# Kernel tuning notes

Hardware: AMD Instinct MI355X
Metric: run time of the kernel (lower is better)

## Reference

```python
import jax, jax.numpy as jnp
import numpy as np

V = 50000      # vocab (embedding table has V+1 rows)
EMB = 256      # emb_dim
E = 128        # rnn_hidden_size (encoder_size)
B, QL, PL, AL = 8, 128, 256, 10


def gru_dir(x, Wih, Whh, bih, bhh, reverse):
    """Single-direction GRU with PyTorch gate math. x: [B,T,I] -> [B,T,H]."""
    pre = jnp.einsum('bti,gi->btg', x, Wih) + bih  # input projection done once: [B,T,3H]
    if reverse:
        pre = pre[:, ::-1]
    H = Whh.shape[1]
    def step(h, p):
        gh = h @ Whh.T + bhh
        r = jax.nn.sigmoid(p[:, :H] + gh[:, :H])
        z = jax.nn.sigmoid(p[:, H:2 * H] + gh[:, H:2 * H])
        n = jnp.tanh(p[:, 2 * H:] + r * gh[:, 2 * H:])
        h_new = (1.0 - z) * n + z * h
        return h_new, h_new
    h0 = jnp.zeros((x.shape[0], H), x.dtype)
    _, hs = jax.lax.scan(step, h0, jnp.swapaxes(pre, 0, 1))
    hs = jnp.swapaxes(hs, 0, 1)
    return hs[:, ::-1] if reverse else hs


def bigru(x, Wih, Whh, bih, bhh):
    f = gru_dir(x, Wih[0], Whh[0], bih[0], bhh[0], False)
    b = gru_dir(x, Wih[1], Whh[1], bih[1], bhh[1], True)
    return jnp.concatenate([f, b], axis=-1)


def setup_inputs() -> dict:
    key = jax.random.key(0)
    ks = iter(jax.random.split(key, 64))
    u = lambda shape, s: jax.random.uniform(next(ks), shape, jnp.float32, -s, s)
    def gru_params(inp, hid):
        s = 1.0 / np.sqrt(hid)
        return (u((2, 3 * hid, inp), s), u((2, 3 * hid, hid), s),
                u((2, 3 * hid), s), u((2, 3 * hid), s))
    d = {}
    d['emb'] = u((V + 1, EMB), 0.1)
    d['a_att'] = u((1, EMB), 0.05)
    for name, (o, i) in {'Wc1': (E, 2 * E), 'Wc2': (E, 2 * E), 'vc': (1, E),
                         'Wb': (2 * E, 2 * E), 'Wd': (E, 2 * E), 'vd': (1, E),
                         'Wm': (E, 2 * E), 'vm': (1, E), 'Ws': (E, 2 * E), 'vs': (1, E),
                         'Wq': (E, 2 * E), 'vq': (1, E), 'Wp1': (E, 2 * E), 'Wp2': (E, 2 * E),
                         'vp': (1, E), 'Wpred': (EMB, 2 * E)}.items():
        d[name] = u((o, i), 0.05)
    d['q_Wih'], d['q_Whh'], d['q_bih'], d['q_bhh'] = gru_params(EMB, E)
    d['p_Wih'], d['p_Whh'], d['p_bih'], d['p_bhh'] = gru_params(EMB, E)
    d['a_Wih'], d['a_Whh'], d['a_bih'], d['a_bhh'] = gru_params(EMB, EMB // 2)
    d['g_Wih'], d['g_Whh'], d['g_bih'], d['g_bhh'] = gru_params(12 * E, E)
    d['query'] = jax.random.randint(next(ks), (B, QL), 0, V)
    d['passage'] = jax.random.randint(next(ks), (B, PL), 0, V)
    d['candidate_neg'] = jax.random.randint(next(ks), (B, AL), 0, V)
    d['candidate_pos'] = jax.random.randint(next(ks), (B, AL), 0, V)
    d['candidate_na'] = jax.random.randint(next(ks), (B, AL), 0, V)
    return d


def reference(emb, a_att, Wc1, Wc2, vc, Wb, Wd, vd, Wm, vm, Ws, vs, Wq, vq, Wp1, Wp2, vp, Wpred,
              q_Wih, q_Whh, q_bih, q_bhh, p_Wih, p_Whh, p_bih, p_bhh,
              a_Wih, a_Whh, a_bih, a_bhh, g_Wih, g_Whh, g_bih, g_bhh,
              query, passage, candidate_neg, candidate_pos, candidate_na):
    def cand_out(ids):
        h = bigru(emb[ids], a_Wih, a_Whh, a_bih, a_bhh)   # [B,A,EMB]
        s = jax.nn.softmax(h @ a_att.T, axis=1)           # softmax over candidate tokens
        return jnp.sum(s * h, axis=1)                     # [B,EMB]
    a_emb = jnp.stack([cand_out(candidate_neg), cand_out(candidate_pos), cand_out(candidate_na)], axis=1)

    # NOTE: source swaps inputs -- q_encoder consumes the passage and vice versa.
    hq = bigru(emb[passage], q_Wih, q_Whh, q_bih, q_bhh)  # [B,P,2E]
    hp = bigru(emb[query], p_Wih, p_Whh, p_bih, p_bhh)    # [B,Q,2E]

    # concat (additive) attention
    sc = jnp.tanh((hq @ Wc1.T)[:, None, :, :] + (hp @ Wc2.T)[:, :, None, :])  # [B,Q,P,E]
    ait = jax.nn.softmax(jnp.einsum('bqpe,e->bqp', sc, vc[0]), axis=-1)
    qtc = jnp.einsum('bqp,bpe->bqe', ait, hq)
    # bilinear attention
    ait = jax.nn.softmax(jnp.einsum('bqe,bpe->bqp', hp, hq @ Wb.T), axis=-1)
    qtb = jnp.einsum('bqp,bpe->bqe', ait, hq)
    # elementwise-product (dot) attention
    prod = hq[:, None, :, :] * hp[:, :, None, :]          # [B,Q,P,2E]
    sd = jnp.tanh(jnp.einsum('bqpf,ef->bqpe', prod, Wd))
    ait = jax.nn.softmax(jnp.einsum('bqpe,e->bqp', sd, vd[0]), axis=-1)
    qtd = jnp.einsum('bqp,bpe->bqe', ait, hq)
    # difference (minus) attention
    diff = hq[:, None, :, :] - hp[:, :, None, :]
    sm = jnp.tanh(jnp.einsum('bqpf,ef->bqpe', diff, Wm))
    ait = jax.nn.softmax(jnp.einsum('bqpe,e->bqp', sm, vm[0]), axis=-1)
    qtm = jnp.einsum('bqp,bpe->bqe', ait, hq)
    # self attention over hp
    sp = hp[:, None, :, :] * hp[:, :, None, :]            # [B,Q,Q,2E]
    ss = jnp.tanh(jnp.einsum('bqkf,ef->bqke', sp, Ws))
    ait = jax.nn.softmax(jnp.einsum('bqke,e->bqk', ss, vs[0]), axis=-1)
    qts = jnp.einsum('bqk,bke->bqe', ait, hp)

    agg = jnp.concatenate([hp, qts, qtc, qtd, qtb, qtm], axis=-1)  # [B,Q,12E]
    agg_rep = bigru(agg, g_Wih, g_Whh, g_bih, g_bhh)               # [B,Q,2E]

    # prediction layer
    sj = jax.nn.softmax(jnp.einsum('bpe,e->bp', jnp.tanh(hq @ Wq.T), vq[0]), axis=-1)
    rq = jnp.einsum('bp,bpe->be', sj, hq)                          # [B,2E]
    # NB: source has no tanh here (vp(Wp1(agg)+Wp2(rq)))
    sj2 = jax.nn.softmax(jnp.einsum('bqe,e->bq', agg_rep @ Wp1.T + (rq @ Wp2.T)[:, None, :], vp[0]), axis=-1)
    rp = jnp.einsum('bq,bqe->be', sj2, agg_rep)                    # [B,2E]
    enc_out = jax.nn.leaky_relu(rp @ Wpred.T)                      # [B,EMB], slope 0.01 as in torch
    logits = jnp.einsum('bce,be->bc', a_emb, enc_out)              # [B,3]
    return logits
```

## Files before the change

### kernel.cpp

```cpp
#include <hip/hip_runtime.h>
#include <hip/hip_bf16.h>


#define BB 8
#define QL 128
#define PL 256
#define AL 10
#define EE 128
#define EMB 256
#define G3 384
#define HH 128

#define O_XPASS   ((size_t)0)
#define O_XQUERY  ((size_t)524288)
#define O_XCAND   ((size_t)786432)
#define O_PREQ    ((size_t)847872)
#define O_PREP    ((size_t)2420736)
#define O_PREA    ((size_t)3207168)
#define O_PREG    ((size_t)3391488)
#define O_HQ      ((size_t)4177920)
#define O_HP      ((size_t)4702208)
#define O_HCAND   ((size_t)4964352)
#define O_AEMB    ((size_t)5025792)
#define O_AQ      ((size_t)5031936)
#define O_AP      ((size_t)5294080)
#define O_BQ      ((size_t)5425152)
#define O_AGG     ((size_t)5949440)
#define O_AGGREP  ((size_t)7522304)
#define O_CQ      ((size_t)7784448)
#define O_GP      ((size_t)8046592)
#define O_RQ      ((size_t)8177664)
#define O_RQW     ((size_t)8179712)
#define O_RP      ((size_t)8180736)
#define O_SCD0    O_XPASS
#define O_SCD1    (O_XPASS + (size_t)262144)
#define O_MQ2     O_PREQ
#define O_MP2     (O_PREQ + (size_t)262144)
#define O_SCS0    O_PREP
#define O_SCS1    (O_PREP + (size_t)131072)

typedef __attribute__((ext_vector_type(8))) short bf16x8;
typedef __attribute__((ext_vector_type(4))) float f32x4;
typedef __attribute__((ext_vector_type(2))) float v2f;
union U4 { uint4 u; bf16x8 v; };

#define BAR_LDS() asm volatile("s_waitcnt lgkmcnt(0)\n\ts_barrier" ::: "memory")

__device__ __forceinline__ float dpp_xadd12(float x){
    int a = __builtin_amdgcn_update_dpp(0, __float_as_int(x), 0xB1, 0xF, 0xF, true);
    x += __int_as_float(a);
    int b = __builtin_amdgcn_update_dpp(0, __float_as_int(x), 0x4E, 0xF, 0xF, true);
    x += __int_as_float(b);
    return x;
}

__device__ __forceinline__ float tanh_fast(float x){
    x = fminf(fmaxf(x, -20.f), 20.f);
    float e = __expf(2.f * x);
    return (e - 1.f) / (e + 1.f);
}
__device__ __forceinline__ float sig_fast(float x){
    return 1.f / (1.f + __expf(-x));
}
__device__ __forceinline__ unsigned pk2(float a, float b){
    unsigned ua = __float_as_uint(a), ub = __float_as_uint(b);
    return ((ua + 0x8000u) >> 16) | ((ub + 0x8000u) & 0xffff0000u);
}

__device__ __forceinline__ void softmax256(float* sc, float* red, int tid){
    float v = sc[tid];
    red[tid] = v;
    __syncthreads();
    for (int s = 128; s > 0; s >>= 1){
        if (tid < s) red[tid] = fmaxf(red[tid], red[tid + s]);
        __syncthreads();
    }
    float m = red[0];
    __syncthreads();
    float e = __expf(v - m);
    red[tid] = e;
    __syncthreads();
    for (int s = 128; s > 0; s >>= 1){
        if (tid < s) red[tid] += red[tid + s];
        __syncthreads();
    }
    float inv = 1.f / red[0];
    __syncthreads();
    sc[tid] = e * inv;
    __syncthreads();
}

__global__ __launch_bounds__(256) void k_gather_all(const int* __restrict__ passage,
                                                    const int* __restrict__ query,
                                                    const int* __restrict__ cneg,
                                                    const int* __restrict__ cpos,
                                                    const int* __restrict__ cna,
                                                    const float* __restrict__ emb,
                                                    float* __restrict__ ws){
    int blk = blockIdx.x, e = threadIdx.x;
    const int* ids; size_t dst; int i;
    if (blk < 2048){            ids = passage; dst = O_XPASS;            i = blk; }
    else if (blk < 3072){       ids = query;   dst = O_XQUERY;           i = blk - 2048; }
    else if (blk < 3152){       ids = cneg;    dst = O_XCAND + 0*20480;  i = blk - 3072; }
    else if (blk < 3232){       ids = cpos;    dst = O_XCAND + 1*20480;  i = blk - 3152; }
    else {                      ids = cna;     dst = O_XCAND + 2*20480;  i = blk - 3232; }
    int id = ids[i];
    ws[dst + (size_t)i * EMB + e] = emb[(size_t)id * EMB + e];
}

__global__ __launch_bounds__(256) void k_gemm_v2(const float* __restrict__ A,
                                                 const float* __restrict__ Bm,
                                                 const float* __restrict__ bias,
                                                 float* __restrict__ C,
                                                 int M, int N, int K,
                                                 long long strideB, long long strideC,
                                                 long long strideBias, int zmode){
    int z = blockIdx.z;
    if (zmode == 0){
        Bm += (size_t)z * strideB;
        C  += (size_t)z * strideC;
        if (bias) bias += (size_t)z * strideBias;
    } else {
        int cc = z >> 1, d = z & 1;
        A  += (size_t)cc * 20480;
        C  += (size_t)cc * 61440 + (size_t)d * strideC;
        Bm += (size_t)d * strideB;
        if (bias) bias += (size_t)d * strideBias;
    }

    __shared__ float As[32][68];
    __shared__ float Bs[32][68];

    int tid = threadIdx.x;
    int i = tid & 15;
    int j = tid >> 4;
    int m0 = blockIdx.y * 64;
    int n0 = blockIdx.x * 64;

    int sm = tid & 63;
    int sk = (tid >> 6) * 8;

    float acc[4][4];
    #pragma unroll
    for (int r = 0; r < 4; ++r)
        #pragma unroll
        for (int c = 0; c < 4; ++c) acc[r][c] = 0.f;

    for (int k0 = 0; k0 < K; k0 += 32){
        float4 a0 = make_float4(0,0,0,0), a1 = make_float4(0,0,0,0);
        if (m0 + sm < M){
            const float* ap = A + (size_t)(m0 + sm) * K + k0 + sk;
            a0 = *(const float4*)ap;
            a1 = *(const float4*)(ap + 4);
        }
        As[sk+0][sm] = a0.x; As[sk+1][sm] = a0.y; As[sk+2][sm] = a0.z; As[sk+3][sm] = a0.w;
        As[sk+4][sm] = a1.x; As[sk+5][sm] = a1.y; As[sk+6][sm] = a1.z; As[sk+7][sm] = a1.w;
        {
            const float* bp = Bm + (size_t)(n0 + sm) * K + k0 + sk;
            float4 b0 = *(const float4*)bp;
            float4 b1 = *(const float4*)(bp + 4);
            Bs[sk+0][sm] = b0.x; Bs[sk+1][sm] = b0.y; Bs[sk+2][sm] = b0.z; Bs[sk+3][sm] = b0.w;
            Bs[sk+4][sm] = b1.x; Bs[sk+5][sm] = b1.y; Bs[sk+6][sm] = b1.z; Bs[sk+7][sm] = b1.w;
        }
        __syncthreads();
        #pragma unroll
        for (int f = 0; f < 32; ++f){
            float4 av = *(const float4*)&As[f][i*4];
            float4 bv = *(const float4*)&Bs[f][j*4];
            float ar[4] = {av.x, av.y, av.z, av.w};
            float bc[4] = {bv.x, bv.y, bv.z, bv.w};
            #pragma unroll
            for (int r = 0; r < 4; ++r)
                #pragma unroll
                for (int c = 0; c < 4; ++c)
                    acc[r][c] += ar[r] * bc[c];
        }
        __syncthreads();
    }

    float4 bv = make_float4(0,0,0,0);
    if (bias) bv = *(const float4*)&bias[n0 + j*4];
    #pragma unroll
    for (int r = 0; r < 4; ++r){
        int row = m0 + i*4 + r;
        if (row < M){
            float4 o;
            o.x = acc[r][0] + bv.x;
            o.y = acc[r][1] + bv.y;
            o.z = acc[r][2] + bv.z;
            o.w = acc[r][3] + bv.w;
            *(float4*)&C[(size_t)row * N + n0 + j*4] = o;
        }
    }
}

#define HSTRIDE 40
__device__ __forceinline__ void gru_body(const float* __restrict__ pre,
                                         const float* __restrict__ Whh,
                                         const float* __restrict__ bhh,
                                         float* __restrict__ out,
                                         int T, int b, int d){
    int tid = threadIdx.x;
    int j = tid >> 2, q = tid & 3;
    int cb = q * 32;

    v2f wr2[16], wz2[16], wn2[16];
    const float* wb = Whh + (size_t)d * G3 * HH;
    {
        const float4* pr4 = (const float4*)(wb + (size_t)j * HH + cb);
        const float4* pz4 = (const float4*)(wb + (size_t)(HH + j) * HH + cb);
        const float4* pn4 = (const float4*)(wb + (size_t)(2*HH + j) * HH + cb);
        #pragma unroll
        for (int kk = 0; kk < 8; ++kk){
            float4 ur = pr4[kk], uz = pz4[kk], un = pn4[kk];
            wr2[2*kk]   = (v2f){ur.x, ur.y}; wr2[2*kk+1] = (v2f){ur.z, ur.w};
            wz2[2*kk]   = (v2f){uz.x, uz.y}; wz2[2*kk+1] = (v2f){uz.z, uz.w};
            wn2[2*kk]   = (v2f){un.x, un.y}; wn2[2*kk+1] = (v2f){un.z, un.w};
        }
    }
    const float* bb = bhh + d * G3;
    float br = bb[j], bz = bb[HH + j], bn = bb[2*HH + j];

    __shared__ __align__(16) float h_s[2][4*HSTRIDE];
    if (tid < 4*HSTRIDE) h_s[0][tid] = 0.f;
    float hprev = 0.f;

    const float* ptB = pre + ((size_t)d * BB + b) * (size_t)T * G3;
    float* ob = out + (size_t)b * T * 256 + d * HH;

    int hw = (j >> 5) * HSTRIDE + (j & 31);

    const float* pt0 = ptB + (size_t)(d ? (T-1) : 0) * G3;
    float pr = pt0[j], pz = pt0[HH + j], pn = pt0[2*HH + j];
    BAR_LDS();

    for (int step = 0; step < T; ++step){
        int t = d ? (T-1-step) : step;
        float nr = 0.f, nz = 0.f, nn = 0.f;
        if (step + 1 < T){
            const float* ptn = ptB + (size_t)(d ? (T-2-step) : (step+1)) * G3;
            nr = ptn[j]; nz = ptn[HH + j]; nn = ptn[2*HH + j];
        }
        int rb = step & 1;
        const float4* h4 = (const float4*)&h_s[rb][q * HSTRIDE];
        v2f ar2 = {0.f,0.f}, az2 = {0.f,0.f}, an2 = {0.f,0.f};
        #pragma unroll
        for (int kk = 0; kk < 8; ++kk){
            float4 hv = h4[kk];
            v2f h0 = {hv.x, hv.y}, h1 = {hv.z, hv.w};
            ar2 += wr2[2*kk] * h0; ar2 += wr2[2*kk+1] * h1;
            az2 += wz2[2*kk] * h0; az2 += wz2[2*kk+1] * h1;
            an2 += wn2[2*kk] * h0; an2 += wn2[2*kk+1] * h1;
        }
        float ar = dpp_xadd12(ar2.x + ar2.y);
        float az = dpp_xadd12(az2.x + az2.y);
        float an = dpp_xadd12(an2.x + an2.y);

        float r = sig_fast(pr + ar + br);
        float z = sig_fast(pz + az + bz);
        float n = tanh_fast(pn + r * (an + bn));
        float h = n + z * (hprev - n);
        hprev = h;

        if (q == 0) h_s[1-rb][hw] = h;
        if (q == 1) ob[(size_t)t * 256 + j] = h;
        pr = nr; pz = nz; pn = nn;
        BAR_LDS();
    }
}

__global__ __launch_bounds__(512, 1) void k_gru_fwd(float* __restrict__ ws,
                                                    const float* __restrict__ qW, const float* __restrict__ qB,
                                                    const float* __restrict__ pW, const float* __restrict__ pB,
                                                    const float* __restrict__ aW, const float* __restrict__ aB){
    int blk = blockIdx.x;
    const float *pre, *W, *bb; float* out; int T, bd;
    if (blk < 16){
        pre = ws + O_PREQ; out = ws + O_HQ; W = qW; bb = qB; T = 256; bd = blk;
    } else if (blk < 32){
        pre = ws + O_PREP; out = ws + O_HP; W = pW; bb = pB; T = 128; bd = blk - 16;
    } else {
        int local = blk - 32; int c = local >> 4;
        pre = ws + O_PREA + (size_t)c * 61440; out = ws + O_HCAND + (size_t)c * 20480;
        W = aW; bb = aB; T = 10; bd = local & 15;
    }
    gru_body(pre, W, bb, out, T, bd >> 1, bd & 1);
}

__global__ __launch_bounds__(512, 1) void k_gru_scan(const float* __restrict__ pre,
                                                     const float* __restrict__ Whh,
                                                     const float* __restrict__ bhh,
                                                     float* __restrict__ out, int T){
    int bd = blockIdx.x & 15;
    gru_body(pre, Whh, bhh, out, T, bd >> 1, bd & 1);
}

__global__ __launch_bounds__(256) void k_cand_att(const float* __restrict__ h,
                                                  const float* __restrict__ a_att,
                                                  float* __restrict__ a_emb){
    int c = blockIdx.x / BB, b = blockIdx.x % BB, tid = threadIdx.x;
    __shared__ float att[256], sc[AL], sw[AL];
    att[tid] = a_att[tid];
    __syncthreads();
    const float* hb = h + (size_t)c * (BB*AL*256) + (size_t)b * (AL*256);
    if (tid < AL){
        float s = 0.f;
        for (int e = 0; e < 256; ++e) s += hb[tid*256 + e] * att[e];
        sc[tid] = s;
    }
    __syncthreads();
    if (tid == 0){
        float m = -1e30f;
        for (int t = 0; t < AL; ++t) m = fmaxf(m, sc[t]);
        float s = 0.f;
        for (int t = 0; t < AL; ++t){ sw[t] = __expf(sc[t] - m); s += sw[t]; }
        float inv = 1.f / s;
        for (int t = 0; t < AL; ++t) sw[t] *= inv;
    }
    __syncthreads();
    float o = 0.f;
    for (int t = 0; t < AL; ++t) o += sw[t] * hb[t*256 + tid];
    a_emb[((size_t)b*3 + c) * 256 + tid] = o;
}

__global__ __launch_bounds__(256, 1) void k_dms_mfma(const float* __restrict__ kv, int P,
                                                     const float* __restrict__ Wmat,
                                                     const float* __restrict__ v,
                                                     const float* __restrict__ xsrc,
                                                     int qPerBlock,
                                                     float* __restrict__ sc){
    int pt = blockIdx.x, qc = blockIdx.y, b = blockIdx.z;
    int tid = threadIdx.x;
    int w = tid >> 6, lane = tid & 63, m = lane & 15, quad = lane >> 4;

    __shared__ unsigned Hlds[64 * 132];
    __shared__ float hpq[256];

    {
        const float* hr = kv + ((size_t)b * P + pt * 64 + w * 16 + m) * 256;
        unsigned* dst = &Hlds[(w * 16 + m) * 132];
        #pragma unroll
        for (int k0 = 0; k0 < 8; ++k0){
            const float* p0 = hr + k0 * 32 + quad * 8;
            float4 x0 = *(const float4*)p0;
            float4 x1 = *(const float4*)(p0 + 4);
            uint4 u;
            u.x = pk2(x0.x, x0.y); u.y = pk2(x0.z, x0.w);
            u.z = pk2(x1.x, x1.y); u.w = pk2(x1.z, x1.w);
            *(uint4*)&dst[k0 * 16 + quad * 4] = u;
        }
    }

    bf16x8 bfr[4][8];
    #pragma unroll
    for (int et = 0; et < 4; ++et){
        const float* wr = Wmat + (size_t)(et * 16 + m) * 256;
        #pragma unroll
        for (int k0 = 0; k0 < 8; ++k0){
            const float* p0 = wr + k0 * 32 + quad * 8;
            float4 x0 = *(const float4*)p0;
            float4 x1 = *(const float4*)(p0 + 4);
            U4 uu;
            uu.u.x = pk2(x0.x, x0.y); uu.u.y = pk2(x0.z, x0.w);
            uu.u.z = pk2(x1.x, x1.y); uu.u.w = pk2(x1.z, x1.w);
            bfr[et][k0] = uu.v;
        }
    }
    float vreg[4];
    #pragma unroll
    for (int et = 0; et < 4; ++et) vreg[et] = v[et * 16 + m];

    __syncthreads();

    const unsigned* hrow = &Hlds[(w * 16 + m) * 132];

    for (int qi = 0; qi < qPerBlock; ++qi){
        int q = qc * qPerBlock + qi;
        __syncthreads();
        hpq[tid] = xsrc[((size_t)b * QL + q) * 256 + tid];
        __syncthreads();

        bf16x8 afr[8];
        #pragma unroll
        for (int k0 = 0; k0 < 8; ++k0){
            uint4 hv = *(const uint4*)&hrow[k0 * 16 + quad * 4];
            const float* hf = &hpq[k0 * 32 + quad * 8];
            float f0 = __uint_as_float(hv.x << 16)         * hf[0];
            float f1 = __uint_as_float(hv.x & 0xffff0000u) * hf[1];
            float f2 = __uint_as_float(hv.y << 16)         * hf[2];
            float f3 = __uint_as_float(hv.y & 0xffff0000u) * hf[3];
            float f4 = __uint_as_float(hv.z << 16)         * hf[4];
            float f5 = __uint_as_float(hv.z & 0xffff0000u) * hf[5];
            float f6 = __uint_as_float(hv.w << 16)         * hf[6];
            float f7 = __uint_as_float(hv.w & 0xffff0000u) * hf[7];
            U4 uu;
            uu.u.x = pk2(f0, f1); uu.u.y = pk2(f2, f3);
            uu.u.z = pk2(f4, f5); uu.u.w = pk2(f6, f7);
            afr[k0] = uu.v;
        }

        f32x4 acc[4];
        #pragma unroll
        for (int et = 0; et < 4; ++et){
            acc[et][0] = 0.f; acc[et][1] = 0.f; acc[et][2] = 0.f; acc[et][3] = 0.f;
        }
        #pragma unroll
        for (int k0 = 0; k0 < 8; ++k0)
            #pragma unroll
            for (int et = 0; et < 4; ++et)
                acc[et] = __builtin_amdgcn_mfma_f32_16x16x32_bf16(afr[k0], bfr[et][k0], acc[et], 0, 0, 0);

        float p0 = 0.f, p1 = 0.f, p2 = 0.f, p3 = 0.f;
        #pragma unroll
        for (int et = 0; et < 4; ++et){
            p0 += vreg[et] * tanh_fast(acc[et][0]);
            p1 += vreg[et] * tanh_fast(acc[et][1]);
            p2 += vreg[et] * tanh_fast(acc[et][2]);
            p3 += vreg[et] * tanh_fast(acc[et][3]);
        }
        p0 = dpp_xadd12(p0); p0 += __shfl_xor(p0, 4); p0 += __shfl_xor(p0, 8);
        p1 = dpp_xadd12(p1); p1 += __shfl_xor(p1, 4); p1 += __shfl_xor(p1, 8);
        p2 = dpp_xadd12(p2); p2 += __shfl_xor(p2, 4); p2 += __shfl_xor(p2, 8);
        p3 = dpp_xadd12(p3); p3 += __shfl_xor(p3, 4); p3 += __shfl_xor(p3, 8);
        if (m == 0){
            float4 o = make_float4(p0, p1, p2, p3);
            *(float4*)&sc[((size_t)b * QL + q) * P + pt * 64 + w * 16 + quad * 4] = o;
        }
    }
}

__global__ __launch_bounds__(256) void k_att_fused(const float* __restrict__ Aqc,
                                                   const float* __restrict__ Apc,
                                                   const float* __restrict__ vc,
                                                   const float* __restrict__ Mq,
                                                   const float* __restrict__ Mp,
                                                   const float* __restrict__ vm,
                                                   const float* __restrict__ Bq,
                                                   const float* __restrict__ scd0,
                                                   const float* __restrict__ scd1,
                                                   const float* __restrict__ scs0,
                                                   const float* __restrict__ scs1,
                                                   const float* __restrict__ hq,
                                                   const float* __restrict__ hp,
                                                   float* __restrict__ agg){
    int b = blockIdx.x >> 7, q = blockIdx.x & 127, tid = threadIdx.x;
    __shared__ float apc[EE], apm[EE], vcs[EE], vms[EE], hpr[256];
    __shared__ float wc[256], wm[256], wbv[256], wd[256], wsx[256];
    __shared__ float sred[2][4][5];

    if (tid < EE){
        apc[tid] = Apc[((size_t)b*QL + q)*EE + tid];
        apm[tid] = Mp [((size_t)b*QL + q)*EE + tid];
        vcs[tid] = vc[tid];
        vms[tid] = vm[tid];
    }
    float hv = hp[((size_t)b*QL + q)*256 + tid];
    hpr[tid] = hv;
    agg[((size_t)b*QL + q)*1536 + tid] = hv;
    __syncthreads();

    int p = tid;
    {
        const float4* a4 = (const float4*)(Aqc + ((size_t)b*PL + p)*EE);
        float s = 0.f;
        #pragma unroll 4
        for (int e4 = 0; e4 < EE/4; ++e4){
            float4 a = a4[e4];
            int e = e4*4;
            s += vcs[e+0] * tanh_fast(a.x + apc[e+0]);
            s += vcs[e+1] * tanh_fast(a.y + apc[e+1]);
            s += vcs[e+2] * tanh_fast(a.z + apc[e+2]);
            s += vcs[e+3] * tanh_fast(a.w + apc[e+3]);
        }
        wc[tid] = s;
    }
    {
        const float4* a4 = (const float4*)(Mq + ((size_t)b*PL + p)*EE);
        float s = 0.f;
        #pragma unroll 4
        for (int e4 = 0; e4 < EE/4; ++e4){
            float4 a = a4[e4];
            int e = e4*4;
            s += vms[e+0] * tanh_fast(a.x - apm[e+0]);
            s += vms[e+1] * tanh_fast(a.y - apm[e+1]);
            s += vms[e+2] * tanh_fast(a.z - apm[e+2]);
            s += vms[e+3] * tanh_fast(a.w - apm[e+3]);
        }
        wm[tid] = s;
    }
    {
        const float4* b4 = (const float4*)(Bq + ((size_t)b*PL + p)*256);
        float s = 0.f;
        #pragma unroll 4
        for (int e4 = 0; e4 < 64; ++e4){
            float4 v = b4[e4];
            int e = e4*4;
            s += hpr[e+0]*v.x; s += hpr[e+1]*v.y;
            s += hpr[e+2]*v.z; s += hpr[e+3]*v.w;
        }
        wbv[tid] = s;
    }
    {
        size_t si = ((size_t)b*QL + q)*PL + tid;
        wd[tid] = scd0[si] + scd1[si];
    }
    {
        if (tid < QL){
            size_t si = ((size_t)b*QL + q)*QL + tid;
            wsx[tid] = scs0[si] + scs1[si];
        } else {
            wsx[tid] = -1e30f;
        }
    }
    __syncthreads();

    {
        int wid = tid >> 6, lane = tid & 63;
        float sv[5] = {wc[tid], wm[tid], wbv[tid], wd[tid], wsx[tid]};
        float mx[5], ex[5];
        #pragma unroll
        for (int i = 0; i < 5; ++i){
            float m = sv[i];
            #pragma unroll
            for (int k = 32; k >= 1; k >>= 1) m = fmaxf(m, __shfl_xor(m, k));
            mx[i] = m;
        }
        if (lane == 0){
            #pragma unroll
            for (int i = 0; i < 5; ++i) sred[0][wid][i] = mx[i];
        }
        __syncthreads();
        #pragma unroll
        for (int i = 0; i < 5; ++i){
            float m = fmaxf(fmaxf(sred[0][0][i], sred[0][1][i]),
                            fmaxf(sred[0][2][i], sred[0][3][i]));
            ex[i] = __expf(sv[i] - m);
            float s = ex[i];
            #pragma unroll
            for (int k = 32; k >= 1; k >>= 1) s += __shfl_xor(s, k);
            mx[i] = s;
        }
        if (lane == 0){
            #pragma unroll
            for (int i = 0; i < 5; ++i) sred[1][wid][i] = mx[i];
        }
        __syncthreads();
        #pragma unroll
        for (int i = 0; i < 5; ++i){
            float s = sred[1][0][i] + sred[1][1][i] + sred[1][2][i] + sred[1][3][i];
            ex[i] *= (1.f / s);
        }
        wc[tid] = ex[0]; wm[tid] = ex[1]; wbv[tid] = ex[2]; wd[tid] = ex[3]; wsx[tid] = ex[4];
        __syncthreads();
    }

    float oc = 0.f, om = 0.f, ob = 0.f, od = 0.f;
    const float* hqb = hq + (size_t)b*PL*256;
    #pragma unroll 4
    for (int pp = 0; pp < PL; ++pp){
        float v = hqb[(size_t)pp*256 + tid];
        oc += wc[pp]  * v;
        om += wm[pp]  * v;
        ob += wbv[pp] * v;
        od += wd[pp]  * v;
    }
    float os = 0.f;
    const float* hpb = hp + (size_t)b*QL*256;
    #pragma unroll 4
    for (int k = 0; k < QL; ++k) os += wsx[k] * hpb[(size_t)k*256 + tid];

    float* ag = agg + ((size_t)b*QL + q)*1536;
    ag[ 256 + tid] = os;
    ag[ 512 + tid] = oc;
    ag[ 768 + tid] = od;
    ag[1024 + tid] = ob;
    ag[1280 + tid] = om;
}

__global__ __launch_bounds__(256) void k_q_att(const float* __restrict__ Cq,
                                               const float* __restrict__ vq,
                                               const float* __restrict__ hq,
                                               float* __restrict__ rq){
    int b = blockIdx.x, tid = threadIdx.x;
    __shared__ float vv[EE], sc[256], red[256];
    if (tid < EE) vv[tid] = vq[tid];
    __syncthreads();
    const float4* c4 = (const float4*)(Cq + ((size_t)b*PL + tid)*EE);
    float s = 0.f;
    #pragma unroll 4
    for (int e4 = 0; e4 < EE/4; ++e4){
        float4 a = c4[e4];
        int e = e4*4;
        s += vv[e+0]*tanh_fast(a.x); s += vv[e+1]*tanh_fast(a.y);
        s += vv[e+2]*tanh_fast(a.z); s += vv[e+3]*tanh_fast(a.w);
    }
    sc[tid] = s;
    __syncthreads();
    softmax256(sc, red, tid);
    float o = 0.f;
    const float* hqb = hq + (size_t)b*PL*256;
    for (int p = 0; p < PL; ++p) o += sc[p] * hqb[(size_t)p*256 + tid];
    rq[(size_t)b*256 + tid] = o;
}

__global__ __launch_bounds__(256) void k_p_att(const float* __restrict__ Gp,
                                               const float* __restrict__ vp,
                                               const float* __restrict__ rqW,
                                               const float* __restrict__ agg_rep,
                                               float* __restrict__ rp){
    int b = blockIdx.x, tid = threadIdx.x;
    __shared__ float vv[EE], rw[EE], sc[256], red[256];
    if (tid < EE){
        vv[tid] = vp[tid];
        rw[tid] = rqW[(size_t)b*EE + tid];
    }
    if (tid >= 128) sc[tid] = -1e30f;
    __syncthreads();
    if (tid < QL){
        const float* gp = Gp + ((size_t)b*QL + tid)*EE;
        float s = 0.f;
        for (int e = 0; e < EE; ++e) s += vv[e] * (gp[e] + rw[e]);
        sc[tid] = s;
    }
    __syncthreads();
    softmax256(sc, red, tid);
    float o = 0.f;
    const float* ab = agg_rep + (size_t)b*QL*256;
    for (int q = 0; q < QL; ++q) o += sc[q] * ab[(size_t)q*256 + tid];
    rp[(size_t)b*256 + tid] = o;
}

__global__ __launch_bounds__(256) void k_final(const float* __restrict__ rp,
                                               const float* __restrict__ Wpred,
                                               const float* __restrict__ a_emb,
                                               float* __restrict__ out){
    int b = blockIdx.x, tid = threadIdx.x;
    __shared__ float rpv[256], enc[256];
    rpv[tid] = rp[(size_t)b*256 + tid];
    __syncthreads();
    const float* wr = Wpred + (size_t)tid*256;
    float s = 0.f;
    #pragma unroll 4
    for (int e = 0; e < 256; ++e) s += wr[e] * rpv[e];
    enc[tid] = (s > 0.f) ? s : 0.01f * s;
    __syncthreads();
    if (tid < 3){
        const float* ae = a_emb + ((size_t)b*3 + tid)*256;
        float o = 0.f;
        for (int e = 0; e < 256; ++e) o += ae[e] * enc[e];
        out[b*3 + tid] = o;
    }
}

extern "C" void kernel_launch(void* const* d_in, const int* in_sizes, int n_in,
                              void* d_out, int out_size, void* d_ws, size_t ws_size,
                              hipStream_t stream){
    const float* emb   = (const float*)d_in[0];
    const float* a_att = (const float*)d_in[1];
    const float* Wc1   = (const float*)d_in[2];
    const float* Wc2   = (const float*)d_in[3];
    const float* vc    = (const float*)d_in[4];
    const float* Wb    = (const float*)d_in[5];
    const float* Wd    = (const float*)d_in[6];
    const float* vd    = (const float*)d_in[7];
    const float* Wm    = (const float*)d_in[8];
    const float* vm    = (const float*)d_in[9];
    const float* Ws    = (const float*)d_in[10];
    const float* vs    = (const float*)d_in[11];
    const float* Wq    = (const float*)d_in[12];
    const float* vq    = (const float*)d_in[13];
    const float* Wp1   = (const float*)d_in[14];
    const float* Wp2   = (const float*)d_in[15];
    const float* vp    = (const float*)d_in[16];
    const float* Wpred = (const float*)d_in[17];
    const float* q_Wih = (const float*)d_in[18];
    const float* q_Whh = (const float*)d_in[19];
    const float* q_bih = (const float*)d_in[20];
    const float* q_bhh = (const float*)d_in[21];
    const float* p_Wih = (const float*)d_in[22];
    const float* p_Whh = (const float*)d_in[23];
    const float* p_bih = (const float*)d_in[24];
    const float* p_bhh = (const float*)d_in[25];
    const float* a_Wih = (const float*)d_in[26];
    const float* a_Whh = (const float*)d_in[27];
    const float* a_bih = (const float*)d_in[28];
    const float* a_bhh = (const float*)d_in[29];
    const float* g_Wih = (const float*)d_in[30];
    const float* g_Whh = (const float*)d_in[31];
    const float* g_bih = (const float*)d_in[32];
    const float* g_bhh = (const float*)d_in[33];
    const int* query   = (const int*)d_in[34];
    const int* passage = (const int*)d_in[35];
    const int* cneg    = (const int*)d_in[36];
    const int* cpos    = (const int*)d_in[37];
    const int* cna     = (const int*)d_in[38];

    float* ws = (float*)d_ws;

    k_gather_all<<<3312, 256, 0, stream>>>(passage, query, cneg, cpos, cna, emb, ws);

    k_gemm_v2<<<dim3(6,32,2), 256, 0, stream>>>(ws+O_XPASS, q_Wih, q_bih, ws+O_PREQ,
                                                2048, 384, 256, 98304LL, 786432LL, 384LL, 0);
    k_gemm_v2<<<dim3(6,16,2), 256, 0, stream>>>(ws+O_XQUERY, p_Wih, p_bih, ws+O_PREP,
                                                1024, 384, 256, 98304LL, 393216LL, 384LL, 0);
    k_gemm_v2<<<dim3(6,2,6), 256, 0, stream>>>(ws+O_XCAND, a_Wih, a_bih, ws+O_PREA,
                                               80, 384, 256, 98304LL, 30720LL, 384LL, 1);

    k_gru_fwd<<<80, 512, 0, stream>>>(ws, q_Whh, q_bhh, p_Whh, p_bhh, a_Whh, a_bhh);

    k_cand_att<<<24, 256, 0, stream>>>(ws+O_HCAND, a_att, ws+O_AEMB);

    k_gemm_v2<<<dim3(2,32,1), 256, 0, stream>>>(ws+O_HQ, Wc1, nullptr, ws+O_AQ,  2048,128,256, 0,0,0, 0);
    k_gemm_v2<<<dim3(2,16,1), 256, 0, stream>>>(ws+O_HP, Wc2, nullptr, ws+O_AP,  1024,128,256, 0,0,0, 0);
    k_gemm_v2<<<dim3(4,32,1), 256, 0, stream>>>(ws+O_HQ, Wb,  nullptr, ws+O_BQ,  2048,256,256, 0,0,0, 0);
    k_gemm_v2<<<dim3(2,32,1), 256, 0, stream>>>(ws+O_HQ, Wq,  nullptr, ws+O_CQ,  2048,128,256, 0,0,0, 0);
    k_gemm_v2<<<dim3(2,32,1), 256, 0, stream>>>(ws+O_HQ, Wm,  nullptr, ws+O_MQ2, 2048,128,256, 0,0,0, 0);
    k_gemm_v2<<<dim3(2,16,1), 256, 0, stream>>>(ws+O_HP, Wm,  nullptr, ws+O_MP2, 1024,128,256, 0,0,0, 0);

    k_dms_mfma<<<dim3(4,8,8), 256, 0, stream>>>(ws+O_HQ, 256, Wd,         vd,    ws+O_HP, 16, ws+O_SCD0);
    k_dms_mfma<<<dim3(4,8,8), 256, 0, stream>>>(ws+O_HQ, 256, Wd + 16384, vd+64, ws+O_HP, 16, ws+O_SCD1);
    k_dms_mfma<<<dim3(2,16,8), 256, 0, stream>>>(ws+O_HP, 128, Ws,         vs,    ws+O_HP, 8, ws+O_SCS0);
    k_dms_mfma<<<dim3(2,16,8), 256, 0, stream>>>(ws+O_HP, 128, Ws + 16384, vs+64, ws+O_HP, 8, ws+O_SCS1);

    k_att_fused<<<1024, 256, 0, stream>>>(ws+O_AQ, ws+O_AP, vc,
                                          ws+O_MQ2, ws+O_MP2, vm,
                                          ws+O_BQ,
                                          ws+O_SCD0, ws+O_SCD1,
                                          ws+O_SCS0, ws+O_SCS1,
                                          ws+O_HQ, ws+O_HP, ws+O_AGG);

    k_gemm_v2<<<dim3(6,16,2), 256, 0, stream>>>(ws+O_AGG, g_Wih, g_bih, ws+O_PREG,
                                                1024, 384, 1536, 589824LL, 393216LL, 384LL, 0);
    k_gru_scan<<<16, 512, 0, stream>>>(ws+O_PREG, g_Whh, g_bhh, ws+O_AGGREP, 128);

    k_q_att<<<8, 256, 0, stream>>>(ws+O_CQ, vq, ws+O_HQ, ws+O_RQ);
    k_gemm_v2<<<dim3(2,16,1), 256, 0, stream>>>(ws+O_AGGREP, Wp1, nullptr, ws+O_GP, 1024,128,256, 0,0,0, 0);
    k_gemm_v2<<<dim3(2,1,1),  256, 0, stream>>>(ws+O_RQ, Wp2, nullptr, ws+O_RQW, 8,128,256, 0,0,0, 0);
    k_p_att<<<8, 256, 0, stream>>>(ws+O_GP, vp, ws+O_RQW, ws+O_AGGREP, ws+O_RP);
    k_final<<<8, 256, 0, stream>>>(ws+O_RP, Wpred, ws+O_AEMB, (float*)d_out);
}
```

Before: 967.2 us.

## Merge independent GEMMs and attention kernels into fewer launches

Independent kernel launches are grouped into combined kernels that dispatch on block index: the input projections, the six attention projections plus candidate attention, the four dms score kernels, the q-attention merged into the fused attention kernel, and the Wp1/Wp2 projections. This cuts launch count from about 22 to 11, which should reduce launch overhead and fill more CUs per launch. The att_fused block mapping is also changed from b-major to b-minor ordering. Shared memory is reused across roles within a kernel, so occupancy follows the largest role's footprint.

```diff
diff --git a/kernel.cpp b/kernel.cpp
--- a/kernel.cpp
+++ b/kernel.cpp
@@ -108,35 +108,16 @@
     ws[dst + (size_t)i * EMB + e] = emb[(size_t)id * EMB + e];
 }
 
-__global__ __launch_bounds__(256) void k_gemm_v2(const float* __restrict__ A,
-                                                 const float* __restrict__ Bm,
-                                                 const float* __restrict__ bias,
-                                                 float* __restrict__ C,
-                                                 int M, int N, int K,
-                                                 long long strideB, long long strideC,
-                                                 long long strideBias, int zmode){
-    int z = blockIdx.z;
-    if (zmode == 0){
-        Bm += (size_t)z * strideB;
-        C  += (size_t)z * strideC;
-        if (bias) bias += (size_t)z * strideBias;
-    } else {
-        int cc = z >> 1, d = z & 1;
-        A  += (size_t)cc * 20480;
-        C  += (size_t)cc * 61440 + (size_t)d * strideC;
-        Bm += (size_t)d * strideB;
-        if (bias) bias += (size_t)d * strideBias;
-    }
-
-    __shared__ float As[32][68];
-    __shared__ float Bs[32][68];
-
+__device__ __forceinline__ void gemm_core(const float* __restrict__ A,
+                                          const float* __restrict__ Bm,
+                                          const float* __restrict__ bias,
+                                          float* __restrict__ C,
+                                          int M, int N, int K, int m0, int n0,
+                                          float (* __restrict__ As)[68],
+                                          float (* __restrict__ Bs)[68]){
     int tid = threadIdx.x;
     int i = tid & 15;
     int j = tid >> 4;
-    int m0 = blockIdx.y * 64;
-    int n0 = blockIdx.x * 64;
-
     int sm = tid & 63;
     int sk = (tid >> 6) * 8;
 
@@ -192,6 +173,44 @@
             *(float4*)&C[(size_t)row * N + n0 + j*4] = o;
         }
     }
+}
+
+__global__ __launch_bounds__(256) void k_pre_all(float* __restrict__ ws,
+        const float* __restrict__ qW, const float* __restrict__ qb,
+        const float* __restrict__ pW, const float* __restrict__ pb,
+        const float* __restrict__ aW, const float* __restrict__ ab){
+    __shared__ float As[32][68];
+    __shared__ float Bs[32][68];
+    int blk = blockIdx.x;
+    if (blk < 384){
+        int z = blk & 1, t = blk >> 1;
+        int my = t / 6, nx = t % 6;
+        gemm_core(ws+O_XPASS, qW + (size_t)z*98304, qb + z*384,
+                  ws+O_PREQ + (size_t)z*786432, 2048, 384, 256, my*64, nx*64, As, Bs);
+    } else if (blk < 576){
+        int u = blk - 384; int z = u & 1, t = u >> 1;
+        int my = t / 6, nx = t % 6;
+        gemm_core(ws+O_XQUERY, pW + (size_t)z*98304, pb + z*384,
+                  ws+O_PREP + (size_t)z*393216, 1024, 384, 256, my*64, nx*64, As, Bs);
+    } else {
+        int u = blk - 576;
+        int nx = u % 6, my = (u/6) & 1, zz = u / 12;
+        int cc = zz >> 1, d = zz & 1;
+        gemm_core(ws+O_XCAND + (size_t)cc*20480, aW + (size_t)d*98304, ab + d*384,
+                  ws+O_PREA + (size_t)cc*61440 + (size_t)d*30720,
+                  80, 384, 256, my*64, nx*64, As, Bs);
+    }
+}
+
+__global__ __launch_bounds__(256) void k_gemm_agg(const float* __restrict__ A,
+                                                  const float* __restrict__ Bm,
+                                                  const float* __restrict__ bias,
+                                                  float* __restrict__ C){
+    __shared__ float As[32][68];
+    __shared__ float Bs[32][68];
+    int z = blockIdx.z;
+    gemm_core(A, Bm + (size_t)z*589824, bias + z*384, C + (size_t)z*393216,
+              1024, 384, 1536, blockIdx.y*64, blockIdx.x*64, As, Bs);
 }
 
 #define HSTRIDE 40
@@ -295,11 +314,14 @@
     gru_body(pre, Whh, bhh, out, T, bd >> 1, bd & 1);
 }
 
-__global__ __launch_bounds__(256) void k_cand_att(const float* __restrict__ h,
-                                                  const float* __restrict__ a_att,
-                                                  float* __restrict__ a_emb){
-    int c = blockIdx.x / BB, b = blockIdx.x % BB, tid = threadIdx.x;
-    __shared__ float att[256], sc[AL], sw[AL];
+__device__ __forceinline__ void cand_att_core(const float* __restrict__ h,
+                                              const float* __restrict__ a_att,
+                                              float* __restrict__ a_emb,
+                                              int u, float* sm){
+    int c = u / BB, b = u % BB, tid = threadIdx.x;
+    float* att = sm;
+    float* sc  = sm + 256;
+    float* sw  = sm + 256 + 16;
     att[tid] = a_att[tid];
     __syncthreads();
     const float* hb = h + (size_t)c * (BB*AL*256) + (size_t)b * (AL*256);
@@ -323,18 +345,61 @@
     a_emb[((size_t)b*3 + c) * 256 + tid] = o;
 }
 
-__global__ __launch_bounds__(256, 1) void k_dms_mfma(const float* __restrict__ kv, int P,
-                                                     const float* __restrict__ Wmat,
-                                                     const float* __restrict__ v,
-                                                     const float* __restrict__ xsrc,
-                                                     int qPerBlock,
-                                                     float* __restrict__ sc){
-    int pt = blockIdx.x, qc = blockIdx.y, b = blockIdx.z;
+__global__ __launch_bounds__(256) void k_proj_all(float* __restrict__ ws,
+        const float* __restrict__ Wc1, const float* __restrict__ Wc2,
+        const float* __restrict__ Wb_, const float* __restrict__ Wq_,
+        const float* __restrict__ Wm_, const float* __restrict__ a_att){
+    __shared__ float As[32][68];
+    __shared__ float Bs[32][68];
+    int blk = blockIdx.x;
+    if (blk < 64){
+        int my = blk >> 1, nx = blk & 1;
+        gemm_core(ws+O_HQ, Wc1, nullptr, ws+O_AQ, 2048,128,256, my*64, nx*64, As, Bs);
+    } else if (blk < 96){
+        int u = blk-64; int my = u >> 1, nx = u & 1;
+        gemm_core(ws+O_HP, Wc2, nullptr, ws+O_AP, 1024,128,256, my*64, nx*64, As, Bs);
+    } else if (blk < 224){
+        int u = blk-96; int my = u >> 2, nx = u & 3;
+        gemm_core(ws+O_HQ, Wb_, nullptr, ws+O_BQ, 2048,256,256, my*64, nx*64, As, Bs);
+    } else if (blk < 288){
+        int u = blk-224; int my = u >> 1, nx = u & 1;
+        gemm_core(ws+O_HQ, Wq_, nullptr, ws+O_CQ, 2048,128,256, my*64, nx*64, As, Bs);
+    } else if (blk < 352){
+        int u = blk-288; int my = u >> 1, nx = u & 1;
+        gemm_core(ws+O_HQ, Wm_, nullptr, ws+O_MQ2, 2048,128,256, my*64, nx*64, As, Bs);
+    } else if (blk < 384){
+        int u = blk-352; int my = u >> 1, nx = u & 1;
+        gemm_core(ws+O_HP, Wm_, nullptr, ws+O_MP2, 1024,128,256, my*64, nx*64, As, Bs);
+    } else {
+        cand_att_core(ws+O_HCAND, a_att, ws+O_AEMB, blk-384, (float*)As);
+    }
+}
+
+__global__ __launch_bounds__(256) void k_fin2(float* __restrict__ ws,
+                                              const float* __restrict__ Wp1,
+                                              const float* __restrict__ Wp2){
+    __shared__ float As[32][68];
+    __shared__ float Bs[32][68];
+    int blk = blockIdx.x;
+    if (blk < 32){
+        int my = blk >> 1, nx = blk & 1;
+        gemm_core(ws+O_AGGREP, Wp1, nullptr, ws+O_GP, 1024,128,256, my*64, nx*64, As, Bs);
+    } else {
+        int nx = blk - 32;
+        gemm_core(ws+O_RQ, Wp2, nullptr, ws+O_RQW, 8,128,256, 0, nx*64, As, Bs);
+    }
+}
+
+__device__ __forceinline__ void dms_core(const float* __restrict__ kv, int P,
+                                         const float* __restrict__ Wmat,
+                                         const float* __restrict__ v,
+                                         const float* __restrict__ xsrc,
+                                         int qPerBlock, float* __restrict__ sc,
+                                         int pt, int qc, int b,
+                                         unsigned* __restrict__ Hlds,
+                                         float* __restrict__ hpq){
     int tid = threadIdx.x;
     int w = tid >> 6, lane = tid & 63, m = lane & 15, quad = lane >> 4;
-
-    __shared__ unsigned Hlds[64 * 132];
-    __shared__ float hpq[256];
 
     {
         const float* hr = kv + ((size_t)b * P + pt * 64 + w * 16 + m) * 256;
@@ -429,6 +494,52 @@
     }
 }
 
+__global__ __launch_bounds__(256, 1) void k_dms_all(float* __restrict__ ws,
+        const float* __restrict__ Wd, const float* __restrict__ vd,
+        const float* __restrict__ Ws_, const float* __restrict__ vs_){
+    __shared__ unsigned Hlds[64 * 132];
+    __shared__ float hpq[256];
+    int blk = blockIdx.x;
+    if (blk < 512){
+        int h = blk >> 8, u = blk & 255;
+        int pt = u & 3, qc = (u >> 2) & 7, b = u >> 5;
+        dms_core(ws+O_HQ, 256, Wd + h*16384, vd + h*64, ws+O_HP, 16,
+                 ws + (h ? O_SCD1 : O_SCD0), pt, qc, b, Hlds, hpq);
+    } else {
+        int v2 = blk - 512;
+        int h = v2 >> 8, u = v2 & 255;
+        int pt = u & 1, qc = (u >> 1) & 15, b = u >> 5;
+        dms_core(ws+O_HP, 128, Ws_ + h*16384, vs_ + h*64, ws+O_HP, 8,
+                 ws + (h ? O_SCS1 : O_SCS0), pt, qc, b, Hlds, hpq);
+    }
+}
+
+__device__ __forceinline__ void q_att_core(const float* __restrict__ Cq,
+                                           const float* __restrict__ vq,
+                                           const float* __restrict__ hq,
+                                           float* __restrict__ rq,
+                                           int b, float* vv, float* sc, float* red){
+    int tid = threadIdx.x;
+    if (tid < EE) vv[tid] = vq[tid];
+    __syncthreads();
+    const float4* c4 = (const float4*)(Cq + ((size_t)b*PL + tid)*EE);
+    float s = 0.f;
+    #pragma unroll 4
+    for (int e4 = 0; e4 < EE/4; ++e4){
+        float4 a = c4[e4];
+        int e = e4*4;
+        s += vv[e+0]*tanh_fast(a.x); s += vv[e+1]*tanh_fast(a.y);
+        s += vv[e+2]*tanh_fast(a.z); s += vv[e+3]*tanh_fast(a.w);
+    }
+    sc[tid] = s;
+    __syncthreads();
+    softmax256(sc, red, tid);
+    float o = 0.f;
+    const float* hqb = hq + (size_t)b*PL*256;
+    for (int p = 0; p < PL; ++p) o += sc[p] * hqb[(size_t)p*256 + tid];
+    rq[(size_t)b*256 + tid] = o;
+}
+
 __global__ __launch_bounds__(256) void k_att_fused(const float* __restrict__ Aqc,
                                                    const float* __restrict__ Apc,
                                                    const float* __restrict__ vc,
@@ -442,11 +553,20 @@
                                                    const float* __restrict__ scs1,
                                                    const float* __restrict__ hq,
                                                    const float* __restrict__ hp,
-                                                   float* __restrict__ agg){
-    int b = blockIdx.x >> 7, q = blockIdx.x & 127, tid = threadIdx.x;
+                                                   float* __restrict__ agg,
+                                                   const float* __restrict__ Cq,
+                                                   const float* __restrict__ vq,
+                                                   float* __restrict__ rq){
     __shared__ float apc[EE], apm[EE], vcs[EE], vms[EE], hpr[256];
     __shared__ float wc[256], wm[256], wbv[256], wd[256], wsx[256];
     __shared__ float sred[2][4][5];
+
+    if (blockIdx.x >= 1024){
+        q_att_core(Cq, vq, hq, rq, blockIdx.x - 1024, apc, wc, wm);
+        return;
+    }
+
+    int b = blockIdx.x & 7, q = blockIdx.x >> 3, tid = threadIdx.x;
 
     if (tid < EE){
         apc[tid] = Apc[((size_t)b*QL + q)*EE + tid];
@@ -575,32 +695,6 @@
     ag[ 768 + tid] = od;
     ag[1024 + tid] = ob;
     ag[1280 + tid] = om;
-}
-
-__global__ __launch_bounds__(256) void k_q_att(const float* __restrict__ Cq,
-                                               const float* __restrict__ vq,
-                                               const float* __restrict__ hq,
-                                               float* __restrict__ rq){
-    int b = blockIdx.x, tid = threadIdx.x;
-    __shared__ float vv[EE], sc[256], red[256];
-    if (tid < EE) vv[tid] = vq[tid];
-    __syncthreads();
-    const float4* c4 = (const float4*)(Cq + ((size_t)b*PL + tid)*EE);
-    float s = 0.f;
-    #pragma unroll 4
-    for (int e4 = 0; e4 < EE/4; ++e4){
-        float4 a = c4[e4];
-        int e = e4*4;
-        s += vv[e+0]*tanh_fast(a.x); s += vv[e+1]*tanh_fast(a.y);
-        s += vv[e+2]*tanh_fast(a.z); s += vv[e+3]*tanh_fast(a.w);
-    }
-    sc[tid] = s;
-    __syncthreads();
-    softmax256(sc, red, tid);
-    float o = 0.f;
-    const float* hqb = hq + (size_t)b*PL*256;
-    for (int p = 0; p < PL; ++p) o += sc[p] * hqb[(size_t)p*256 + tid];
-    rq[(size_t)b*256 + tid] = o;
 }
 
 __global__ __launch_bounds__(256) void k_p_att(const float* __restrict__ Gp,
@@ -699,43 +793,26 @@
 
     k_gather_all<<<3312, 256, 0, stream>>>(passage, query, cneg, cpos, cna, emb, ws);
 
-    k_gemm_v2<<<dim3(6,32,2), 256, 0, stream>>>(ws+O_XPASS, q_Wih, q_bih, ws+O_PREQ,
-                                                2048, 384, 256, 98304LL, 786432LL, 384LL, 0);
-    k_gemm_v2<<<dim3(6,16,2), 256, 0, stream>>>(ws+O_XQUERY, p_Wih, p_bih, ws+O_PREP,
-                                                1024, 384, 256, 98304LL, 393216LL, 384LL, 0);
-    k_gemm_v2<<<dim3(6,2,6), 256, 0, stream>>>(ws+O_XCAND, a_Wih, a_bih, ws+O_PREA,
-                                               80, 384, 256, 98304LL, 30720LL, 384LL, 1);
+    k_pre_all<<<648, 256, 0, stream>>>(ws, q_Wih, q_bih, p_Wih, p_bih, a_Wih, a_bih);
 
     k_gru_fwd<<<80, 512, 0, stream>>>(ws, q_Whh, q_bhh, p_Whh, p_bhh, a_Whh, a_bhh);
 
-    k_cand_att<<<24, 256, 0, stream>>>(ws+O_HCAND, a_att, ws+O_AEMB);
-
-    k_gemm_v2<<<dim3(2,32,1), 256, 0, stream>>>(ws+O_HQ, Wc1, nullptr, ws+O_AQ,  2048,128,256, 0,0,0, 0);
-    k_gemm_v2<<<dim3(2,16,1), 256, 0, stream>>>(ws+O_HP, Wc2, nullptr, ws+O_AP,  1024,128,256, 0,0,0, 0);
-    k_gemm_v2<<<dim3(4,32,1), 256, 0, stream>>>(ws+O_HQ, Wb,  nullptr, ws+O_BQ,  2048,256,256, 0,0,0, 0);
-    k_gemm_v2<<<dim3(2,32,1), 256, 0, stream>>>(ws+O_HQ, Wq,  nullptr, ws+O_CQ,  2048,128,256, 0,0,0, 0);
-    k_gemm_v2<<<dim3(2,32,1), 256, 0, stream>>>(ws+O_HQ, Wm,  nullptr, ws+O_MQ2, 2048,128,256, 0,0,0, 0);
-    k_gemm_v2<<<dim3(2,16,1), 256, 0, stream>>>(ws+O_HP, Wm,  nullptr, ws+O_MP2, 1024,128,256, 0,0,0, 0);
-
-    k_dms_mfma<<<dim3(4,8,8), 256, 0, stream>>>(ws+O_HQ, 256, Wd,         vd,    ws+O_HP, 16, ws+O_SCD0);
-    k_dms_mfma<<<dim3(4,8,8), 256, 0, stream>>>(ws+O_HQ, 256, Wd + 16384, vd+64, ws+O_HP, 16, ws+O_SCD1);
-    k_dms_mfma<<<dim3(2,16,8), 256, 0, stream>>>(ws+O_HP, 128, Ws,         vs,    ws+O_HP, 8, ws+O_SCS0);
-    k_dms_mfma<<<dim3(2,16,8), 256, 0, stream>>>(ws+O_HP, 128, Ws + 16384, vs+64, ws+O_HP, 8, ws+O_SCS1);
-
-    k_att_fused<<<1024, 256, 0, stream>>>(ws+O_AQ, ws+O_AP, vc,
+    k_proj_all<<<408, 256, 0, stream>>>(ws, Wc1, Wc2, Wb, Wq, Wm, a_att);
+
+    k_dms_all<<<1024, 256, 0, stream>>>(ws, Wd, vd, Ws, vs);
+
+    k_att_fused<<<1032, 256, 0, stream>>>(ws+O_AQ, ws+O_AP, vc,
                                           ws+O_MQ2, ws+O_MP2, vm,
                                           ws+O_BQ,
                                           ws+O_SCD0, ws+O_SCD1,
                                           ws+O_SCS0, ws+O_SCS1,
-                                          ws+O_HQ, ws+O_HP, ws+O_AGG);
-
-    k_gemm_v2<<<dim3(6,16,2), 256, 0, stream>>>(ws+O_AGG, g_Wih, g_bih, ws+O_PREG,
-                                                1024, 384, 1536, 589824LL, 393216LL, 384LL, 0);
+                                          ws+O_HQ, ws+O_HP, ws+O_AGG,
+                                          ws+O_CQ, vq, ws+O_RQ);
+
+    k_gemm_agg<<<dim3(6,16,2), 256, 0, stream>>>(ws+O_AGG, g_Wih, g_bih, ws+O_PREG);
     k_gru_scan<<<16, 512, 0, stream>>>(ws+O_PREG, g_Whh, g_bhh, ws+O_AGGREP, 128);
 
-    k_q_att<<<8, 256, 0, stream>>>(ws+O_CQ, vq, ws+O_HQ, ws+O_RQ);
-    k_gemm_v2<<<dim3(2,16,1), 256, 0, stream>>>(ws+O_AGGREP, Wp1, nullptr, ws+O_GP, 1024,128,256, 0,0,0, 0);
-    k_gemm_v2<<<dim3(2,1,1),  256, 0, stream>>>(ws+O_RQ, Wp2, nullptr, ws+O_RQW, 8,128,256, 0,0,0, 0);
+    k_fin2<<<34, 256, 0, stream>>>(ws, Wp1, Wp2);
     k_p_att<<<8, 256, 0, stream>>>(ws+O_GP, vp, ws+O_RQW, ws+O_AGGREP, ws+O_RP);
     k_final<<<8, 256, 0, stream>>>(ws+O_RP, Wpred, ws+O_AEMB, (float*)d_out);
 }
```

Result: faster. 777.7 us (-19.6%).
